# Performance work log

Measured on AMD Instinct MI355X. Metric: run time of the kernel, lower is better.

The kernel has to match this reference:

```python
import jax, jax.numpy as jnp
import numpy as np

B, N, C = 4, 2048, 128
H = 4
HD = C // H
SCALE = HD ** -0.5
NEG = -9e15


def setup_inputs() -> dict:
    key = jax.random.key(0)
    ks = jax.random.split(key, 6)
    x = jax.random.normal(ks[0], (B, N, C), dtype=jnp.float32)
    A = jax.random.randint(ks[1], (N, N), 0, 2, dtype=jnp.int32)
    std = 0.02
    Wq = jax.random.normal(ks[2], (C, C), dtype=jnp.float32) * std
    Wkv = jax.random.normal(ks[3], (2 * C, C), dtype=jnp.float32) * std
    Wp = jax.random.normal(ks[4], (C, C), dtype=jnp.float32) * std
    bp = jnp.zeros((C,), dtype=jnp.float32)
    return {"x": x, "A": A, "Wq": Wq, "Wkv": Wkv, "Wp": Wp, "bp": bp}


def reference(x, A, Wq, Wkv, Wp, bp):
    # q/k/v projections (torch Linear: x @ W.T)
    q = (x @ Wq.T).reshape(B, N, H, HD).transpose(0, 2, 1, 3)      # [B,H,N,HD]
    kv = (x @ Wkv.T).reshape(B, N, 2, H, HD).transpose(2, 0, 3, 1, 4)
    k, v = kv[0], kv[1]                                            # [B,H,N,HD]
    attn = jnp.einsum('bhnd,bhmd->bhnm', q, k) * SCALE             # [B,H,N,N]
    attn = jnp.where(A > 0, attn, NEG)                             # adjacency mask
    attn = jax.nn.softmax(attn, axis=-1)
    out = jnp.einsum('bhnm,bhmd->bhnd', attn, v)                   # [B,H,N,HD]
    out = out.transpose(0, 2, 1, 3).reshape(B, N, C)
    out = out @ Wp.T + bp
    return out + x                                                 # residual
```

## Files before the change

kernel.cpp:

```cpp
#include <hip/hip_runtime.h>
#include <math.h>

constexpr int kB = 4, kN = 2048, kC = 128, kH = 4, kHD = 32;
constexpr float kScaleLog2e = 0.17677669529663687f * 1.4426950408889634f;

typedef __attribute__((ext_vector_type(8))) short bf16x8;
typedef __attribute__((ext_vector_type(4))) float f32x4;

__device__ __forceinline__ float exp2fast(float v) { return __builtin_amdgcn_exp2f(v); }
__device__ __forceinline__ unsigned int cvtpk(float lo, float hi) {
  unsigned int r;
  asm("v_cvt_pk_bf16_f32 %0, %1, %2" : "=v"(r) : "v"(lo), "v"(hi));
  return r;
}
__device__ __forceinline__ float bflo(unsigned int u) {
  union { unsigned int u; float f; } v; v.u = u << 16; return v.f;
}
__device__ __forceinline__ float bfhi(unsigned int u) {
  union { unsigned int u; float f; } v; v.u = u & 0xFFFF0000u; return v.f;
}

__global__ __launch_bounds__(256) void prep_kernel(
    const int* __restrict__ A, const float* __restrict__ Wq,
    const float* __restrict__ Wkv, const float* __restrict__ Wp,
    unsigned long long* __restrict__ Abits, unsigned short* __restrict__ Wallb,
    unsigned short* __restrict__ Wpb) {
  const int bid = blockIdx.x;
  if (bid < 512) {
    const int lane = threadIdx.x & 63;
    const int w0 = bid * 4 + (threadIdx.x >> 6);
    #pragma unroll 4
    for (int k = 0; k < 32; ++k) {
      const int idx = w0 + k * 2048;
      const int row = idx >> 5, c0 = (idx & 31) * 64;
      unsigned long long msk = __ballot(A[(size_t)row * kN + c0 + lane] > 0);
      if (lane == 0) Abits[idx] = msk;
    }
  } else {
    const int i4 = ((bid - 512) * 256 + threadIdx.x) * 4;
    float4 v;
    unsigned short* dst;
    if (i4 < 16384) {
      v = *(const float4*)&Wq[i4];
      v.x *= kScaleLog2e; v.y *= kScaleLog2e; v.z *= kScaleLog2e; v.w *= kScaleLog2e;
      dst = Wallb + i4;
    } else if (i4 < 49152) {
      v = *(const float4*)&Wkv[i4 - 16384];
      dst = Wallb + i4;
    } else {
      v = *(const float4*)&Wp[i4 - 49152];
      dst = Wpb + (i4 - 49152);
    }
    *(uint2*)dst = make_uint2(cvtpk(v.x, v.y), cvtpk(v.z, v.w));
  }
}

__global__ __launch_bounds__(256) void qkv_kernel(
    const float* __restrict__ x, const unsigned short* __restrict__ Wallb,
    unsigned short* __restrict__ qws, unsigned short* __restrict__ kws,
    unsigned short* __restrict__ vtws) {
  __shared__ unsigned short xs[16][136];
  const int t = threadIdx.x;
  const int row0 = blockIdx.x * 16;
  const int b = row0 >> 11;
  {
    const int r = t >> 4, c = (t & 15) * 8;
    const float* src = x + (size_t)(row0 + r) * kC + c;
    float4 a = *(const float4*)src;
    float4 bb = *(const float4*)(src + 4);
    *(uint4*)&xs[r][c] = make_uint4(cvtpk(a.x, a.y), cvtpk(a.z, a.w),
                                    cvtpk(bb.x, bb.y), cvtpk(bb.z, bb.w));
  }
  __syncthreads();
  const int w = t >> 6, l = t & 63, lr = l & 15, g = l >> 4;
  bf16x8 xf[4];
  #pragma unroll
  for (int s = 0; s < 4; ++s) xf[s] = *(const bf16x8*)&xs[lr][s * 32 + g * 8];
  #pragma unroll
  for (int ci = 0; ci < 6; ++ci) {
    const int c0 = (w * 6 + ci) * 16;
    const unsigned short* wr = Wallb + (size_t)(c0 + lr) * kC + g * 8;
    f32x4 acc = {0.f, 0.f, 0.f, 0.f};
    if (c0 < 256) {
      #pragma unroll
      for (int s = 0; s < 4; ++s) {
        bf16x8 wf = *(const bf16x8*)(wr + s * 32);
        acc = __builtin_amdgcn_mfma_f32_16x16x32_bf16(wf, xf[s], acc, 0, 0, 0);
      }
      const int col0 = c0 + g * 4;
      const int h = (col0 & 127) >> 5, hd0 = col0 & 31;
      unsigned short* dst = (col0 < 128) ? qws : kws;
      uint2 pk = make_uint2(cvtpk(acc[0], acc[1]), cvtpk(acc[2], acc[3]));
      *(uint2*)&dst[((size_t)(b * kH + h) * kN + row0 + lr) * kHD + hd0] = pk;
    } else {
      #pragma unroll
      for (int s = 0; s < 4; ++s) {
        bf16x8 wf = *(const bf16x8*)(wr + s * 32);
        acc = __builtin_amdgcn_mfma_f32_16x16x32_bf16(xf[s], wf, acc, 0, 0, 0);
      }
      const int d = (c0 - 256) + lr;
      uint2 pk = make_uint2(cvtpk(acc[0], acc[1]), cvtpk(acc[2], acc[3]));
      *(uint2*)&vtws[((size_t)(b * kH + (d >> 5)) * kHD + (d & 31)) * kN + row0 + g * 4] = pk;
    }
  }
}

__global__ __launch_bounds__(256) void attn_kernel(
    const unsigned short* __restrict__ qws, const unsigned short* __restrict__ kws,
    const unsigned short* __restrict__ vtws,
    const unsigned long long* __restrict__ Abits,
    unsigned short* __restrict__ Opart, float* __restrict__ lws, int tiles) {
  __shared__ unsigned short Ksf[2][4][64][8];
  __shared__ unsigned short Vtf[2][2][2][64][8];
  __shared__ unsigned short Psf[4][2][2][64][8];
  const int t = threadIdx.x, w = t >> 6, l = t & 63, lr = l & 15, g = l >> 4;
  const int bh = blockIdx.x, qblk = blockIdx.y, z = blockIdx.z;
  const int q0 = qblk * 128;
  const int qa = q0 + w * 32 + lr, qb = qa + 16;
  const int kt0 = z * tiles;
  const unsigned short* kbase = kws + (size_t)bh * kN * kHD;
  const unsigned short* vbase = vtws + (size_t)bh * kHD * kN;
  bf16x8 qf0 = *(const bf16x8*)&qws[((size_t)bh * kN + qa) * kHD + g * 8];
  bf16x8 qf1 = *(const bf16x8*)&qws[((size_t)bh * kN + qb) * kHD + g * 8];
  const unsigned long long* arow0 = Abits + (size_t)qa * (kN / 64);
  const unsigned long long* arow1 = Abits + (size_t)qb * (kN / 64);

  const int skc = t >> 6, sl = t & 63;
  const size_t koff = ((size_t)(skc * 16 + (sl & 15))) * kHD + (sl >> 4) * 8;
  const int sdh = t >> 7, sct = (t >> 6) & 1;
  const size_t voff = ((size_t)(sdh * 16 + (sl & 15))) * kN + sct * 32 + (sl >> 4) * 8;

  bf16x8 kreg = *(const bf16x8*)(kbase + (size_t)kt0 * 64 * kHD + koff);
  bf16x8 vreg = *(const bf16x8*)(vbase + (size_t)kt0 * 64 + voff);
  *(bf16x8*)&Ksf[0][skc][sl][0] = kreg;
  *(bf16x8*)&Vtf[0][sdh][sct][sl][0] = vreg;
  unsigned long long mw0 = arow0[kt0], mw1 = arow1[kt0], mw0n = 0, mw1n = 0;

  f32x4 o0a = {0.f, 0.f, 0.f, 0.f}, o1a = o0a, o2a = o0a;
  f32x4 o0b = o0a, o1b = o0a, o2b = o0a;
  bf16x8 ones;
  #pragma unroll
  for (int i = 0; i < 8; ++i) ones[i] = (short)0x3F80;
  const int gsh = g * 4;
  unsigned short* const psw0 = &Psf[w][0][0][0][0];
  unsigned short* const psw1 = &Psf[w][1][0][0][0];
  const int pbase = (((g >> 1) << 4) | lr) * 8 + (g & 1) * 4;

  #pragma unroll 2
  for (int it = 0; it < tiles; ++it) {
    const int c = it & 1;
    const int kt = kt0 + it;
    __syncthreads();
    if (it + 1 < tiles) {
      kreg = *(const bf16x8*)(kbase + (size_t)(kt + 1) * 64 * kHD + koff);
      vreg = *(const bf16x8*)(vbase + (size_t)(kt + 1) * 64 + voff);
      mw0n = arow0[kt + 1];
      mw1n = arow1[kt + 1];
    }
    const unsigned int wlo0 = ((unsigned int)mw0) >> gsh;
    const unsigned int whi0 = ((unsigned int)(mw0 >> 32)) >> gsh;
    const unsigned int wlo1 = ((unsigned int)mw1) >> gsh;
    const unsigned int whi1 = ((unsigned int)(mw1 >> 32)) >> gsh;

    #pragma unroll
    for (int kc = 0; kc < 4; ++kc) {
      bf16x8 kf = *(const bf16x8*)&Ksf[c][kc][l][0];
      f32x4 z4 = {0.f, 0.f, 0.f, 0.f};
      f32x4 acc0 = __builtin_amdgcn_mfma_f32_16x16x32_bf16(kf, qf0, z4, 0, 0, 0);
      f32x4 acc1 = __builtin_amdgcn_mfma_f32_16x16x32_bf16(kf, qf1, z4, 0, 0, 0);
      const unsigned int word0 = (kc < 2) ? wlo0 : whi0;
      const unsigned int word1 = (kc < 2) ? wlo1 : whi1;
      float p0[4], p1[4];
      #pragma unroll
      for (int i = 0; i < 4; ++i) {
        float e0 = exp2fast(acc0[i]);
        float e1 = exp2fast(acc1[i]);
        int m0, m1;
        asm("v_bfe_i32 %0, %1, %2, 1" : "=v"(m0) : "v"(word0), "n"((kc & 1) * 16 + i));
        asm("v_bfe_i32 %0, %1, %2, 1" : "=v"(m1) : "v"(word1), "n"((kc & 1) * 16 + i));
        union { float f; int u; } u0, u1;
        u0.f = e0; u0.u &= m0; p0[i] = u0.f;
        u1.f = e1; u1.u &= m1; p1[i] = u1.f;
      }
      *(uint2*)(psw0 + kc * 256 + pbase) =
          make_uint2(cvtpk(p0[0], p0[1]), cvtpk(p0[2], p0[3]));
      *(uint2*)(psw1 + kc * 256 + pbase) =
          make_uint2(cvtpk(p1[0], p1[1]), cvtpk(p1[2], p1[3]));
    }
    #pragma unroll
    for (int ct = 0; ct < 2; ++ct) {
      bf16x8 pf0 = *(const bf16x8*)&Psf[w][0][ct][l][0];
      bf16x8 pf1 = *(const bf16x8*)&Psf[w][1][ct][l][0];
      bf16x8 va = *(const bf16x8*)&Vtf[c][0][ct][l][0];
      bf16x8 vb = *(const bf16x8*)&Vtf[c][1][ct][l][0];
      o0a = __builtin_amdgcn_mfma_f32_16x16x32_bf16(va, pf0, o0a, 0, 0, 0);
      o1a = __builtin_amdgcn_mfma_f32_16x16x32_bf16(vb, pf0, o1a, 0, 0, 0);
      o2a = __builtin_amdgcn_mfma_f32_16x16x32_bf16(ones, pf0, o2a, 0, 0, 0);
      o0b = __builtin_amdgcn_mfma_f32_16x16x32_bf16(va, pf1, o0b, 0, 0, 0);
      o1b = __builtin_amdgcn_mfma_f32_16x16x32_bf16(vb, pf1, o1b, 0, 0, 0);
      o2b = __builtin_amdgcn_mfma_f32_16x16x32_bf16(ones, pf1, o2b, 0, 0, 0);
    }
    if (it + 1 < tiles) {
      *(bf16x8*)&Ksf[c ^ 1][skc][sl][0] = kreg;
      *(bf16x8*)&Vtf[c ^ 1][sdh][sct][sl][0] = vreg;
      mw0 = mw0n;
      mw1 = mw1n;
    }
  }

  unsigned short* orow0 = Opart + ((size_t)(z * 16 + bh) * kN + qa) * kHD;
  unsigned short* orow1 = Opart + ((size_t)(z * 16 + bh) * kN + qb) * kHD;
  *(uint2*)&orow0[g * 4]      = make_uint2(cvtpk(o0a[0], o0a[1]), cvtpk(o0a[2], o0a[3]));
  *(uint2*)&orow0[16 + g * 4] = make_uint2(cvtpk(o1a[0], o1a[1]), cvtpk(o1a[2], o1a[3]));
  *(uint2*)&orow1[g * 4]      = make_uint2(cvtpk(o0b[0], o0b[1]), cvtpk(o0b[2], o0b[3]));
  *(uint2*)&orow1[16 + g * 4] = make_uint2(cvtpk(o1b[0], o1b[1]), cvtpk(o1b[2], o1b[3]));
  if (g == 0) {
    lws[(size_t)(z * 16 + bh) * kN + qa] = o2a[0];
    lws[(size_t)(z * 16 + bh) * kN + qb] = o2b[0];
  }
}

__global__ __launch_bounds__(256) void proj_kernel(
    const unsigned short* __restrict__ Opart, const float* __restrict__ lws,
    const unsigned short* __restrict__ Wpb, const float* __restrict__ bp,
    const float* __restrict__ x, float* __restrict__ out, int np) {
  const int t = threadIdx.x, w = t >> 6, l = t & 63, lr = l & 15, g = l >> 4;
  const int row0 = blockIdx.x * 16;
  const int b = row0 >> 11;
  bf16x8 af[4];
  #pragma unroll
  for (int s = 0; s < 4; ++s) {
    const int bh = b * kH + s;
    float a0 = 0.f, a1 = 0.f, a2 = 0.f, a3 = 0.f, a4 = 0.f, a5 = 0.f, a6 = 0.f, a7 = 0.f;
    float lacc = 0.f;
    for (int p = 0; p < np; ++p) {
      const size_t base = (size_t)(p * 16 + bh) * kN + row0 + lr;
      const uint4 u = *(const uint4*)&Opart[base * kHD + g * 8];
      lacc += lws[base];
      a0 += bflo(u.x); a1 += bfhi(u.x);
      a2 += bflo(u.y); a3 += bfhi(u.y);
      a4 += bflo(u.z); a5 += bfhi(u.z);
      a6 += bflo(u.w); a7 += bfhi(u.w);
    }
    const float inv = 1.f / fmaxf(lacc, 1e-30f);
    union { uint4 u; bf16x8 v; } cv;
    cv.u = make_uint4(cvtpk(a0 * inv, a1 * inv), cvtpk(a2 * inv, a3 * inv),
                      cvtpk(a4 * inv, a5 * inv), cvtpk(a6 * inv, a7 * inv));
    af[s] = cv.v;
  }
  #pragma unroll
  for (int ci = 0; ci < 2; ++ci) {
    const int c0 = (w * 2 + ci) * 16;
    const unsigned short* wr = Wpb + (size_t)(c0 + lr) * kC + g * 8;
    f32x4 acc = {0.f, 0.f, 0.f, 0.f};
    #pragma unroll
    for (int s = 0; s < 4; ++s) {
      bf16x8 wf = *(const bf16x8*)(wr + s * 32);
      acc = __builtin_amdgcn_mfma_f32_16x16x32_bf16(wf, af[s], acc, 0, 0, 0);
    }
    const int col0 = c0 + g * 4;
    const size_t off = (size_t)(row0 + lr) * kC + col0;
    const float4 xb = *(const float4*)&x[off];
    const float4 bb = *(const float4*)&bp[col0];
    float4 r;
    r.x = acc[0] + bb.x + xb.x;
    r.y = acc[1] + bb.y + xb.y;
    r.z = acc[2] + bb.z + xb.z;
    r.w = acc[3] + bb.w + xb.w;
    *(float4*)&out[off] = r;
  }
}

extern "C" void kernel_launch(void* const* d_in, const int* in_sizes, int n_in,
                              void* d_out, int out_size, void* d_ws, size_t ws_size,
                              hipStream_t stream) {
  const float* x   = (const float*)d_in[0];
  const int*   A   = (const int*)d_in[1];
  const float* Wq  = (const float*)d_in[2];
  const float* Wkv = (const float*)d_in[3];
  const float* Wp  = (const float*)d_in[4];
  const float* bp  = (const float*)d_in[5];
  float* out = (float*)d_out;
  char* ws = (char*)d_ws;

  unsigned short* qws   = (unsigned short*)(ws);
  unsigned short* kws   = (unsigned short*)(ws + (2u << 20));
  unsigned short* vtws  = (unsigned short*)(ws + (4u << 20));
  unsigned long long* Abits = (unsigned long long*)(ws + (6u << 20));
  unsigned short* Wallb = (unsigned short*)(ws + (6u << 20) + (1u << 19));
  unsigned short* Wpb   = Wallb + 384 * 128;
  float*          lws   = (float*)(ws + (7u << 20));
  unsigned short* Opart = (unsigned short*)(ws + (8u << 20));

  const int np = (ws_size >= (16u << 20)) ? 4 : 1;
  const int tiles = 32 / np;

  prep_kernel<<<dim3(576), dim3(256), 0, stream>>>(A, Wq, Wkv, Wp, Abits, Wallb, Wpb);
  qkv_kernel<<<dim3(512), dim3(256), 0, stream>>>(x, Wallb, qws, kws, vtws);
  attn_kernel<<<dim3(16, 16, np), dim3(256), 0, stream>>>(
      qws, kws, vtws, Abits, Opart, lws, tiles);
  proj_kernel<<<dim3(512), dim3(256), 0, stream>>>(Opart, lws, Wpb, bp, x, out, np);
}
```

Before: 58.89 us.

## Permute K row layout so P stays in registers as PV MFMA operand

Reorders which key rows are loaded into each K fragment slot so that the QK^T MFMA output layout directly matches the B-operand layout needed by the PV MFMA. The probability tile is then packed into registers instead of being written to and read back from the per-wave shared-memory P buffer, and the mask bit extraction offsets are adjusted to the new key permutation. This removes LDS traffic and shared memory footprint per tile, at the cost of more live registers and reliance on a subtle index mapping being correct.

Result: no change. 57.91 us (-1.7%).

```diff
diff --git a/kernel.cpp b/kernel.cpp
--- a/kernel.cpp
+++ b/kernel.cpp
@@ -112,7 +112,6 @@
     unsigned short* __restrict__ Opart, float* __restrict__ lws, int tiles) {
   __shared__ unsigned short Ksf[2][4][64][8];
   __shared__ unsigned short Vtf[2][2][2][64][8];
-  __shared__ unsigned short Psf[4][2][2][64][8];
   const int t = threadIdx.x, w = t >> 6, l = t & 63, lr = l & 15, g = l >> 4;
   const int bh = blockIdx.x, qblk = blockIdx.y, z = blockIdx.z;
   const int q0 = qblk * 128;
@@ -126,7 +125,9 @@
   const unsigned long long* arow1 = Abits + (size_t)qb * (kN / 64);
 
   const int skc = t >> 6, sl = t & 63;
-  const size_t koff = ((size_t)(skc * 16 + (sl & 15))) * kHD + (sl >> 4) * 8;
+  const int srow = sl & 15;
+  const int scol = (skc >> 1) * 32 + (srow >> 2) * 8 + (skc & 1) * 4 + (srow & 3);
+  const size_t koff = (size_t)scol * kHD + (sl >> 4) * 8;
   const int sdh = t >> 7, sct = (t >> 6) & 1;
   const size_t voff = ((size_t)(sdh * 16 + (sl & 15))) * kN + sct * 32 + (sl >> 4) * 8;
 
@@ -141,10 +142,7 @@
   bf16x8 ones;
   #pragma unroll
   for (int i = 0; i < 8; ++i) ones[i] = (short)0x3F80;
-  const int gsh = g * 4;
-  unsigned short* const psw0 = &Psf[w][0][0][0][0];
-  unsigned short* const psw1 = &Psf[w][1][0][0][0];
-  const int pbase = (((g >> 1) << 4) | lr) * 8 + (g & 1) * 4;
+  const int gsh = g * 8;
 
   #pragma unroll 2
   for (int it = 0; it < tiles; ++it) {
@@ -162,6 +160,7 @@
     const unsigned int wlo1 = ((unsigned int)mw1) >> gsh;
     const unsigned int whi1 = ((unsigned int)(mw1 >> 32)) >> gsh;
 
+    unsigned int pk0[2][4], pk1[2][4];
     #pragma unroll
     for (int kc = 0; kc < 4; ++kc) {
       bf16x8 kf = *(const bf16x8*)&Ksf[c][kc][l][0];
@@ -176,29 +175,30 @@
         float e0 = exp2fast(acc0[i]);
         float e1 = exp2fast(acc1[i]);
         int m0, m1;
-        asm("v_bfe_i32 %0, %1, %2, 1" : "=v"(m0) : "v"(word0), "n"((kc & 1) * 16 + i));
-        asm("v_bfe_i32 %0, %1, %2, 1" : "=v"(m1) : "v"(word1), "n"((kc & 1) * 16 + i));
+        asm("v_bfe_i32 %0, %1, %2, 1" : "=v"(m0) : "v"(word0), "n"((kc & 1) * 4 + i));
+        asm("v_bfe_i32 %0, %1, %2, 1" : "=v"(m1) : "v"(word1), "n"((kc & 1) * 4 + i));
         union { float f; int u; } u0, u1;
         u0.f = e0; u0.u &= m0; p0[i] = u0.f;
         u1.f = e1; u1.u &= m1; p1[i] = u1.f;
       }
-      *(uint2*)(psw0 + kc * 256 + pbase) =
-          make_uint2(cvtpk(p0[0], p0[1]), cvtpk(p0[2], p0[3]));
-      *(uint2*)(psw1 + kc * 256 + pbase) =
-          make_uint2(cvtpk(p1[0], p1[1]), cvtpk(p1[2], p1[3]));
+      pk0[kc >> 1][(kc & 1) * 2]     = cvtpk(p0[0], p0[1]);
+      pk0[kc >> 1][(kc & 1) * 2 + 1] = cvtpk(p0[2], p0[3]);
+      pk1[kc >> 1][(kc & 1) * 2]     = cvtpk(p1[0], p1[1]);
+      pk1[kc >> 1][(kc & 1) * 2 + 1] = cvtpk(p1[2], p1[3]);
     }
     #pragma unroll
     for (int ct = 0; ct < 2; ++ct) {
-      bf16x8 pf0 = *(const bf16x8*)&Psf[w][0][ct][l][0];
-      bf16x8 pf1 = *(const bf16x8*)&Psf[w][1][ct][l][0];
+      union { uint4 u; bf16x8 v; } pb0, pb1;
+      pb0.u = make_uint4(pk0[ct][0], pk0[ct][1], pk0[ct][2], pk0[ct][3]);
+      pb1.u = make_uint4(pk1[ct][0], pk1[ct][1], pk1[ct][2], pk1[ct][3]);
       bf16x8 va = *(const bf16x8*)&Vtf[c][0][ct][l][0];
       bf16x8 vb = *(const bf16x8*)&Vtf[c][1][ct][l][0];
-      o0a = __builtin_amdgcn_mfma_f32_16x16x32_bf16(va, pf0, o0a, 0, 0, 0);
-      o1a = __builtin_amdgcn_mfma_f32_16x16x32_bf16(vb, pf0, o1a, 0, 0, 0);
-      o2a = __builtin_amdgcn_mfma_f32_16x16x32_bf16(ones, pf0, o2a, 0, 0, 0);
-      o0b = __builtin_amdgcn_mfma_f32_16x16x32_bf16(va, pf1, o0b, 0, 0, 0);
-      o1b = __builtin_amdgcn_mfma_f32_16x16x32_bf16(vb, pf1, o1b, 0, 0, 0);
-      o2b = __builtin_amdgcn_mfma_f32_16x16x32_bf16(ones, pf1, o2b, 0, 0, 0);
+      o0a = __builtin_amdgcn_mfma_f32_16x16x32_bf16(va, pb0.v, o0a, 0, 0, 0);
+      o1a = __builtin_amdgcn_mfma_f32_16x16x32_bf16(vb, pb0.v, o1a, 0, 0, 0);
+      o2a = __builtin_amdgcn_mfma_f32_16x16x32_bf16(ones, pb0.v, o2a, 0, 0, 0);
+      o0b = __builtin_amdgcn_mfma_f32_16x16x32_bf16(va, pb1.v, o0b, 0, 0, 0);
+      o1b = __builtin_amdgcn_mfma_f32_16x16x32_bf16(vb, pb1.v, o1b, 0, 0, 0);
+      o2b = __builtin_amdgcn_mfma_f32_16x16x32_bf16(ones, pb1.v, o2b, 0, 0, 0);
     }
     if (it + 1 < tiles) {
       *(bf16x8*)&Ksf[c ^ 1][skc][sl][0] = kreg;
```
